# Performance work log

Measured on AMD Instinct MI355X. Metric: run time of the kernel, lower is better.

Reference implementation:

```python
import jax, jax.numpy as jnp
import numpy as np

N_NODES = 50000
N_EDGES = 800000
D = 128


def setup_inputs() -> dict:
    key = jax.random.key(0)
    k1, k2, k3, k4 = jax.random.split(key, 4)
    x = jax.random.normal(k1, (N_NODES, D), dtype=jnp.float32)
    src = jax.random.randint(k2, (N_EDGES,), 0, N_NODES, dtype=jnp.int64)
    dst = jax.random.randint(k3, (N_EDGES,), 0, N_NODES, dtype=jnp.int64)
    # nn.Linear(D, D, bias=False): weight shape [out, in]
    W = jax.random.normal(k4, (D, D), dtype=jnp.float32) * (1.0 / np.sqrt(D))
    return {"x": x, "src": src, "dst": dst, "W": W}


def reference(x, src, dst, W):
    h_in = x
    # update_all(copy_src, reduce_sum): gather src features, segment-sum over dst
    agg = jax.ops.segment_sum(x[src], dst, num_segments=N_NODES)  # [N, D]
    h = agg @ W.T                 # Linear(bias=False)
    h = jax.nn.relu(h)            # activation
    h = h + h_in                  # residual (is_normalize=False)
    return h
```

## Files before the change

kernel.cpp:

```cpp
#include <hip/hip_runtime.h>
#include <hip/hip_bf16.h>

#define N_NODES 50000
#define N_EDGES 800000
#define D 128

#define NBUCK 782
#define BCAP  2048

#define SCAT_BLOCKS ((N_EDGES / 4 + 1023) / 1024)

using bf16x8 = __attribute__((ext_vector_type(8))) short;
using u16x8  = __attribute__((ext_vector_type(8))) unsigned short;
using f32x4  = __attribute__((ext_vector_type(4))) float;

static __device__ __forceinline__ ushort f2bf(float f) {
    __hip_bfloat16 h = __float2bfloat16(f);
    return *reinterpret_cast<ushort*>(&h);
}
static __device__ __forceinline__ float bf2f(ushort u) {
    return __uint_as_float(((unsigned)u) << 16);
}


__global__ void __launch_bounds__(1024)
convert_scatter(const float4* __restrict__ x4, ushort* __restrict__ xb,
                const int* __restrict__ src, const int* __restrict__ dst,
                int* __restrict__ bcnt, int* __restrict__ pairs) {
    __shared__ int lcnt[NBUCK], lbase[NBUCK];
    const int tid = threadIdx.x;
    if (tid < NBUCK) lcnt[tid] = 0;

    const int i = blockIdx.x * 1024 + tid;
    const bool valid = i < N_EDGES / 4;
    int4 s, d;
    if (valid) {
        s = ((const int4*)src)[i];
        d = ((const int4*)dst)[i];
    }

    const int total4 = N_NODES * D / 4;
    const int stride = gridDim.x * 1024;
    for (int j = blockIdx.x * 1024 + tid; j < total4; j += stride) {
        float4 v = x4[j];
        ushort4 u = make_ushort4(f2bf(v.x), f2bf(v.y), f2bf(v.z), f2bf(v.w));
        *(ushort4*)(xb + (size_t)j * 4) = u;
    }
    __syncthreads();

    int bkt[4], slot[4];
    if (valid) {
        bkt[0] = d.x >> 6; slot[0] = atomicAdd(&lcnt[bkt[0]], 1);
        bkt[1] = d.y >> 6; slot[1] = atomicAdd(&lcnt[bkt[1]], 1);
        bkt[2] = d.z >> 6; slot[2] = atomicAdd(&lcnt[bkt[2]], 1);
        bkt[3] = d.w >> 6; slot[3] = atomicAdd(&lcnt[bkt[3]], 1);
    }
    __syncthreads();
    if (tid < NBUCK) {
        int c = lcnt[tid];
        lbase[tid] = c ? atomicAdd(&bcnt[tid], c) : 0;
    }
    __syncthreads();
    if (valid) {
#pragma unroll
        for (int e = 0; e < 4; ++e) {
            int sv = (e == 0) ? s.x : (e == 1) ? s.y : (e == 2) ? s.z : s.w;
            int dv = (e == 0) ? d.x : (e == 1) ? d.y : (e == 2) ? d.z : d.w;
            int pos = lbase[bkt[e]] + slot[e];
            if (pos < BCAP)
                pairs[bkt[e] * BCAP + pos] = sv | ((dv & 63) << 16);
        }
    }
}

__global__ void __launch_bounds__(256)
bucket_to_csr(const int* __restrict__ pairs, const int* __restrict__ bcnt,
              ushort* __restrict__ sorted_u16, int2* __restrict__ off2) {
    __shared__ int lcnt2[64], lcur[64];
    __shared__ ushort lsrc[BCAP];
    const int b    = blockIdx.x;
    const int tid  = threadIdx.x;
    const int base = b * BCAP;
    int n = bcnt[b];
    if (n > BCAP) n = BCAP;

    if (tid < 64) lcnt2[tid] = 0;
    __syncthreads();
    for (int i = tid; i < n; i += 256)
        atomicAdd(&lcnt2[pairs[base + i] >> 16], 1);
    __syncthreads();

    if (tid < 64) {
        int v = lcnt2[tid];
        int incl = v;
#pragma unroll
        for (int o = 1; o < 64; o <<= 1) {
            int t = __shfl_up(incl, o, 64);
            if (tid >= o) incl += t;
        }
        int excl = incl - v;
        lcur[tid] = excl;
        int gn = b * 64 + tid;
        if (gn < N_NODES)
            off2[gn] = make_int2(base + excl, base + incl);
    }
    __syncthreads();
    for (int i = tid; i < n; i += 256) {
        int p = pairs[base + i];
        int pos = atomicAdd(&lcur[p >> 16], 1);
        lsrc[pos] = (ushort)(p & 0xFFFF);
    }
    __syncthreads();
    for (int i = tid; i < n; i += 256)
        sorted_u16[base + i] = lsrc[i];
}

__global__ void __launch_bounds__(256)
gather_sum(const ushort* __restrict__ xb, const ushort* __restrict__ sorted_u16,
           const int2* __restrict__ off2, ushort* __restrict__ aggb) {
    int node = (int)((blockIdx.x * 256 + threadIdx.x) >> 6);
    int lane = threadIdx.x & 63;
    if (node >= N_NODES) return;
    const int q4 = lane >> 4;
    const int c8 = (lane & 15) << 3;
    const ushort* xbb = xb + c8;
    int2 oo = off2[node];
    int beg = oo.x, end = oo.y;

    float acc[8];
#pragma unroll
    for (int j = 0; j < 8; ++j) acc[j] = 0.f;

    for (int base = beg; base < end; base += 64) {
        int n = end - base;
        if (n > 64) n = 64;
        int idx = (lane < n) ? (int)sorted_u16[base + lane] : 0;
        int full = n >> 2;
        int t = 0;
        for (; t + 4 <= full; t += 4) {
            int s0 = __shfl(idx, 4 * t + q4, 64);
            int s1 = __shfl(idx, 4 * t + 4 + q4, 64);
            int s2 = __shfl(idx, 4 * t + 8 + q4, 64);
            int s3 = __shfl(idx, 4 * t + 12 + q4, 64);
            u16x8 u0 = *(const u16x8*)(xbb + (size_t)s0 * D);
            u16x8 u1 = *(const u16x8*)(xbb + (size_t)s1 * D);
            u16x8 u2 = *(const u16x8*)(xbb + (size_t)s2 * D);
            u16x8 u3 = *(const u16x8*)(xbb + (size_t)s3 * D);
#pragma unroll
            for (int j = 0; j < 8; ++j)
                acc[j] += (bf2f(u0[j]) + bf2f(u1[j])) + (bf2f(u2[j]) + bf2f(u3[j]));
        }
        for (; t < full; ++t) {
            int s = __shfl(idx, 4 * t + q4, 64);
            u16x8 u = *(const u16x8*)(xbb + (size_t)s * D);
#pragma unroll
            for (int j = 0; j < 8; ++j) acc[j] += bf2f(u[j]);
        }
        int rem = n & 3;
        if (rem) {
            int s = __shfl(idx, 4 * full + q4, 64);
            if (q4 < rem) {
                u16x8 u = *(const u16x8*)(xbb + (size_t)s * D);
#pragma unroll
                for (int j = 0; j < 8; ++j) acc[j] += bf2f(u[j]);
            }
        }
    }
#pragma unroll
    for (int j = 0; j < 8; ++j) {
        acc[j] += __shfl_xor(acc[j], 16, 64);
        acc[j] += __shfl_xor(acc[j], 32, 64);
    }
    if (q4 == 0) {
        u16x8 u;
#pragma unroll
        for (int j = 0; j < 8; ++j) u[j] = f2bf(acc[j]);
        *(u16x8*)(aggb + (size_t)node * D + c8) = u;
    }
}

__global__ void __launch_bounds__(256)
gemm_relu_res(const ushort* __restrict__ aggb,
              const float* __restrict__ W,
              const ushort* __restrict__ xb,
              float* __restrict__ out) {
    __shared__ __align__(16) char lds[33792];
    ushort* Wl = (ushort*)lds;

    const int tid  = threadIdx.x;
    const int lane = tid & 63;
    const int wv   = tid >> 6;
    const int m16  = lane & 15;
    const int q    = lane >> 4;

#pragma unroll
    for (int i = 0; i < 8; ++i) {
        int g  = tid + i * 256;
        int o  = g & 127;
        int kc = g >> 7;
        const float4* wp = (const float4*)(W + (size_t)o * D + kc * 8);
        float4 w0 = wp[0], w1 = wp[1];
        bf16x8 hv;
        hv[0] = (short)f2bf(w0.x); hv[1] = (short)f2bf(w0.y);
        hv[2] = (short)f2bf(w0.z); hv[3] = (short)f2bf(w0.w);
        hv[4] = (short)f2bf(w1.x); hv[5] = (short)f2bf(w1.y);
        hv[6] = (short)f2bf(w1.z); hv[7] = (short)f2bf(w1.w);
        *(bf16x8*)&Wl[g * 8] = hv;
    }
    __syncthreads();

    const int nb = blockIdx.x * 64 + wv * 16;
    int arow = nb + m16;
    if (arow >= N_NODES) arow = N_NODES - 1;

    bf16x8 a[4];
#pragma unroll
    for (int kb = 0; kb < 4; ++kb)
        a[kb] = *(const bf16x8*)&aggb[(size_t)arow * D + kb * 32 + q * 8];

    f32x4 acc[8];
#pragma unroll
    for (int t = 0; t < 8; ++t) {
        acc[t] = (f32x4){0.f, 0.f, 0.f, 0.f};
#pragma unroll
        for (int kb = 0; kb < 4; ++kb) {
            bf16x8 bfr = *(const bf16x8*)&Wl[(((kb * 4 + q) * 128) + t * 16 + m16) * 8];
            acc[t] = __builtin_amdgcn_mfma_f32_16x16x32_bf16(a[kb], bfr, acc[t], 0, 0, 0);
        }
    }

    __syncthreads();
    float* Ew = (float*)(lds + wv * 8448);
#pragma unroll
    for (int t = 0; t < 8; ++t)
#pragma unroll
        for (int r = 0; r < 4; ++r)
            Ew[(q * 4 + r) * 132 + t * 16 + m16] = acc[t][r];

    const int h  = lane >> 5;
    const int c4 = (lane & 31) << 2;
#pragma unroll
    for (int j = 0; j < 8; ++j) {
        int r = j * 2 + h;
        int node = nb + r;
        if (node < N_NODES) {
            float4 v  = *(const float4*)&Ew[r * 132 + c4];
            ushort4 xu = *(const ushort4*)(xb + (size_t)node * D + c4);
            float4 o;
            o.x = fmaxf(v.x, 0.f) + bf2f(xu.x);
            o.y = fmaxf(v.y, 0.f) + bf2f(xu.y);
            o.z = fmaxf(v.z, 0.f) + bf2f(xu.z);
            o.w = fmaxf(v.w, 0.f) + bf2f(xu.w);
            *(float4*)(out + (size_t)node * D + c4) = o;
        }
    }
}

__global__ void zero_out(float4* __restrict__ p, int n4) {
    int i = blockIdx.x * 256 + threadIdx.x;
    if (i < n4) p[i] = make_float4(0.f, 0.f, 0.f, 0.f);
}
__global__ void scatter_edges(const float* __restrict__ x,
                              const int* __restrict__ src,
                              const int* __restrict__ dst,
                              float* __restrict__ agg) {
    long long tid = (long long)blockIdx.x * 256 + threadIdx.x;
    if (tid >= (long long)N_EDGES * 32) return;
    int edge = (int)(tid >> 5);
    int c    = ((int)tid & 31) << 2;
    const float4 v = *(const float4*)(x + (size_t)src[edge] * D + c);
    float* p = agg + (size_t)dst[edge] * D + c;
    unsafeAtomicAdd(p + 0, v.x);
    unsafeAtomicAdd(p + 1, v.y);
    unsafeAtomicAdd(p + 2, v.z);
    unsafeAtomicAdd(p + 3, v.w);
}
__global__ void __launch_bounds__(256)
gemm_relu_res_f32(float* data, const float* __restrict__ W,
                  const float* __restrict__ x) {
    __shared__ __align__(16) char lds[50176];
    ushort* Wl = (ushort*)lds;
    ushort* Al = (ushort*)(lds + 32768);
    const int tid  = threadIdx.x;
    const int lane = tid & 63;
    const int wv   = tid >> 6;
    const int m16  = lane & 15;
    const int q    = lane >> 4;
#pragma unroll
    for (int i = 0; i < 8; ++i) {
        int g  = tid + i * 256;
        int o  = g & 127;
        int kc = g >> 7;
        const float4* wp = (const float4*)(W + (size_t)o * D + kc * 8);
        float4 w0 = wp[0], w1 = wp[1];
        bf16x8 hv;
        hv[0] = (short)f2bf(w0.x); hv[1] = (short)f2bf(w0.y);
        hv[2] = (short)f2bf(w0.z); hv[3] = (short)f2bf(w0.w);
        hv[4] = (short)f2bf(w1.x); hv[5] = (short)f2bf(w1.y);
        hv[6] = (short)f2bf(w1.z); hv[7] = (short)f2bf(w1.w);
        *(bf16x8*)&Wl[g * 8] = hv;
    }
    __syncthreads();
    const int nb = blockIdx.x * 64 + wv * 16;
    ushort* Aw = &Al[wv * (16 * 136)];
#pragma unroll
    for (int m = 0; m < 16; ++m) {
        int node = nb + m;
        float2 v = make_float2(0.f, 0.f);
        if (node < N_NODES)
            v = *(const float2*)(data + (size_t)node * D + lane * 2);
        *(ushort2*)&Aw[m * 136 + lane * 2] = make_ushort2(f2bf(v.x), f2bf(v.y));
    }
    bf16x8 a[4];
#pragma unroll
    for (int kb = 0; kb < 4; ++kb)
        a[kb] = *(const bf16x8*)&Aw[m16 * 136 + kb * 32 + q * 8];
    f32x4 acc[8];
#pragma unroll
    for (int t = 0; t < 8; ++t) {
        acc[t] = (f32x4){0.f, 0.f, 0.f, 0.f};
#pragma unroll
        for (int kb = 0; kb < 4; ++kb) {
            bf16x8 bfr = *(const bf16x8*)&Wl[(((kb * 4 + q) * 128) + t * 16 + m16) * 8];
            acc[t] = __builtin_amdgcn_mfma_f32_16x16x32_bf16(a[kb], bfr, acc[t], 0, 0, 0);
        }
    }
    __syncthreads();
    float* Ew = (float*)(lds + wv * 8448);
#pragma unroll
    for (int t = 0; t < 8; ++t)
#pragma unroll
        for (int r = 0; r < 4; ++r)
            Ew[(q * 4 + r) * 132 + t * 16 + m16] = acc[t][r];
    const int h  = lane >> 5;
    const int c4 = (lane & 31) << 2;
#pragma unroll
    for (int j = 0; j < 8; ++j) {
        int r = j * 2 + h;
        int node = nb + r;
        if (node < N_NODES) {
            float4 v  = *(const float4*)&Ew[r * 132 + c4];
            float4 xi = *(const float4*)(x + (size_t)node * D + c4);
            float4 o;
            o.x = fmaxf(v.x, 0.f) + xi.x;
            o.y = fmaxf(v.y, 0.f) + xi.y;
            o.z = fmaxf(v.z, 0.f) + xi.z;
            o.w = fmaxf(v.w, 0.f) + xi.w;
            *(float4*)(data + (size_t)node * D + c4) = o;
        }
    }
}

extern "C" void kernel_launch(void* const* d_in, const int* in_sizes, int n_in,
                              void* d_out, int out_size, void* d_ws, size_t ws_size,
                              hipStream_t stream) {
    const float* x   = (const float*)d_in[0];
    const int*   src = (const int*)d_in[1];
    const int*   dst = (const int*)d_in[2];
    const float* W   = (const float*)d_in[3];
    float* out = (float*)d_out;

    char* ws = (char*)d_ws;
    int*    bcnt  = (int*)ws;        ws += (size_t)NBUCK * 4;
    ws = (char*)(((uintptr_t)ws + 15) & ~(uintptr_t)15);
    int*    pairs = (int*)ws;        ws += (size_t)NBUCK * BCAP * 4;
    ushort* su16  = (ushort*)ws;     ws += (size_t)NBUCK * BCAP * 2;
    int2*   off2  = (int2*)ws;       ws += (size_t)N_NODES * 8;
    ws = (char*)(((uintptr_t)ws + 15) & ~(uintptr_t)15);
    ushort* xb    = (ushort*)ws;     ws += (size_t)N_NODES * D * 2;
    ushort* aggb  = (ushort*)ws;     ws += (size_t)N_NODES * D * 2;
    const bool big_ws = (ws_size >= (size_t)(ws - (char*)d_ws));

    if (big_ws) {
        hipMemsetAsync(bcnt, 0, (size_t)NBUCK * 4, stream);
        convert_scatter<<<SCAT_BLOCKS, 1024, 0, stream>>>(
            (const float4*)x, xb, src, dst, bcnt, pairs);
        bucket_to_csr<<<NBUCK, 256, 0, stream>>>(pairs, bcnt, su16, off2);
        gather_sum<<<(N_NODES * 64 + 255) / 256, 256, 0, stream>>>(
            xb, su16, off2, aggb);
        gemm_relu_res<<<(N_NODES + 63) / 64, 256, 0, stream>>>(aggb, W, xb, out);
    } else {
        int n4 = N_NODES * D / 4;
        zero_out<<<(n4 + 255) / 256, 256, 0, stream>>>((float4*)out, n4);
        long long n_scatter = (long long)N_EDGES * 32;
        scatter_edges<<<(int)((n_scatter + 255) / 256), 256, 0, stream>>>(
            x, src, dst, out);
        gemm_relu_res_f32<<<(N_NODES + 63) / 64, 256, 0, stream>>>(out, W, x);
    }
}
```

Baseline: 148.0 us.

## Fuse bucket-to-CSR, neighbor gather and GEMM epilogue into one kernel

```diff
diff --git a/kernel.cpp b/kernel.cpp
--- a/kernel.cpp
+++ b/kernel.cpp
@@ -7,6 +7,7 @@
 
 #define NBUCK 782
 #define BCAP  2048
+#define LCAP  1536
 
 #define SCAT_BLOCKS ((N_EDGES / 4 + 1023) / 1024)
 
@@ -74,119 +75,18 @@
 }
 
 __global__ void __launch_bounds__(256)
-bucket_to_csr(const int* __restrict__ pairs, const int* __restrict__ bcnt,
-              ushort* __restrict__ sorted_u16, int2* __restrict__ off2) {
-    __shared__ int lcnt2[64], lcur[64];
-    __shared__ ushort lsrc[BCAP];
+csr_gather_gemm(const int* __restrict__ pairs, const int* __restrict__ bcnt,
+                const ushort* __restrict__ xb, const float* __restrict__ W,
+                float* __restrict__ out) {
+    __shared__ __align__(16) char lds[54016];
+    ushort* Wl    = (ushort*)lds;
+    ushort* lsrc  = (ushort*)(lds + 32768);
+    ushort* aggL  = (ushort*)(lds + 35840);
+    int*    lcnt2 = (int*)(lds + 53248);
+    int*    lcur  = (int*)(lds + 53504);
+    int*    lbeg  = (int*)(lds + 53760);
+
     const int b    = blockIdx.x;
-    const int tid  = threadIdx.x;
-    const int base = b * BCAP;
-    int n = bcnt[b];
-    if (n > BCAP) n = BCAP;
-
-    if (tid < 64) lcnt2[tid] = 0;
-    __syncthreads();
-    for (int i = tid; i < n; i += 256)
-        atomicAdd(&lcnt2[pairs[base + i] >> 16], 1);
-    __syncthreads();
-
-    if (tid < 64) {
-        int v = lcnt2[tid];
-        int incl = v;
-#pragma unroll
-        for (int o = 1; o < 64; o <<= 1) {
-            int t = __shfl_up(incl, o, 64);
-            if (tid >= o) incl += t;
-        }
-        int excl = incl - v;
-        lcur[tid] = excl;
-        int gn = b * 64 + tid;
-        if (gn < N_NODES)
-            off2[gn] = make_int2(base + excl, base + incl);
-    }
-    __syncthreads();
-    for (int i = tid; i < n; i += 256) {
-        int p = pairs[base + i];
-        int pos = atomicAdd(&lcur[p >> 16], 1);
-        lsrc[pos] = (ushort)(p & 0xFFFF);
-    }
-    __syncthreads();
-    for (int i = tid; i < n; i += 256)
-        sorted_u16[base + i] = lsrc[i];
-}
-
-__global__ void __launch_bounds__(256)
-gather_sum(const ushort* __restrict__ xb, const ushort* __restrict__ sorted_u16,
-           const int2* __restrict__ off2, ushort* __restrict__ aggb) {
-    int node = (int)((blockIdx.x * 256 + threadIdx.x) >> 6);
-    int lane = threadIdx.x & 63;
-    if (node >= N_NODES) return;
-    const int q4 = lane >> 4;
-    const int c8 = (lane & 15) << 3;
-    const ushort* xbb = xb + c8;
-    int2 oo = off2[node];
-    int beg = oo.x, end = oo.y;
-
-    float acc[8];
-#pragma unroll
-    for (int j = 0; j < 8; ++j) acc[j] = 0.f;
-
-    for (int base = beg; base < end; base += 64) {
-        int n = end - base;
-        if (n > 64) n = 64;
-        int idx = (lane < n) ? (int)sorted_u16[base + lane] : 0;
-        int full = n >> 2;
-        int t = 0;
-        for (; t + 4 <= full; t += 4) {
-            int s0 = __shfl(idx, 4 * t + q4, 64);
-            int s1 = __shfl(idx, 4 * t + 4 + q4, 64);
-            int s2 = __shfl(idx, 4 * t + 8 + q4, 64);
-            int s3 = __shfl(idx, 4 * t + 12 + q4, 64);
-            u16x8 u0 = *(const u16x8*)(xbb + (size_t)s0 * D);
-            u16x8 u1 = *(const u16x8*)(xbb + (size_t)s1 * D);
-            u16x8 u2 = *(const u16x8*)(xbb + (size_t)s2 * D);
-            u16x8 u3 = *(const u16x8*)(xbb + (size_t)s3 * D);
-#pragma unroll
-            for (int j = 0; j < 8; ++j)
-                acc[j] += (bf2f(u0[j]) + bf2f(u1[j])) + (bf2f(u2[j]) + bf2f(u3[j]));
-        }
-        for (; t < full; ++t) {
-            int s = __shfl(idx, 4 * t + q4, 64);
-            u16x8 u = *(const u16x8*)(xbb + (size_t)s * D);
-#pragma unroll
-            for (int j = 0; j < 8; ++j) acc[j] += bf2f(u[j]);
-        }
-        int rem = n & 3;
-        if (rem) {
-            int s = __shfl(idx, 4 * full + q4, 64);
-            if (q4 < rem) {
-                u16x8 u = *(const u16x8*)(xbb + (size_t)s * D);
-#pragma unroll
-                for (int j = 0; j < 8; ++j) acc[j] += bf2f(u[j]);
-            }
-        }
-    }
-#pragma unroll
-    for (int j = 0; j < 8; ++j) {
-        acc[j] += __shfl_xor(acc[j], 16, 64);
-        acc[j] += __shfl_xor(acc[j], 32, 64);
-    }
-    if (q4 == 0) {
-        u16x8 u;
-#pragma unroll
-        for (int j = 0; j < 8; ++j) u[j] = f2bf(acc[j]);
-        *(u16x8*)(aggb + (size_t)node * D + c8) = u;
-    }
-}
-
-__global__ void __launch_bounds__(256)
-gemm_relu_res(const ushort* __restrict__ aggb,
-              const float* __restrict__ W,
-              const ushort* __restrict__ xb,
-              float* __restrict__ out) {
-    __shared__ __align__(16) char lds[33792];
-    ushort* Wl = (ushort*)lds;
-
     const int tid  = threadIdx.x;
     const int lane = tid & 63;
     const int wv   = tid >> 6;
@@ -207,16 +107,89 @@
         hv[6] = (short)f2bf(w1.z); hv[7] = (short)f2bf(w1.w);
         *(bf16x8*)&Wl[g * 8] = hv;
     }
-    __syncthreads();
-
-    const int nb = blockIdx.x * 64 + wv * 16;
-    int arow = nb + m16;
-    if (arow >= N_NODES) arow = N_NODES - 1;
+
+    const int base = b * BCAP;
+    int n = bcnt[b];
+    if (n > LCAP) n = LCAP;
+    if (tid < 64) lcnt2[tid] = 0;
+    __syncthreads();
+    for (int i = tid; i < n; i += 256)
+        atomicAdd(&lcnt2[pairs[base + i] >> 16], 1);
+    __syncthreads();
+    if (tid < 64) {
+        int v = lcnt2[tid];
+        int incl = v;
+#pragma unroll
+        for (int o = 1; o < 64; o <<= 1) {
+            int t = __shfl_up(incl, o, 64);
+            if (tid >= o) incl += t;
+        }
+        lbeg[tid] = incl - v;
+        lcur[tid] = incl - v;
+    }
+    __syncthreads();
+    for (int i = tid; i < n; i += 256) {
+        int p = pairs[base + i];
+        int pos = atomicAdd(&lcur[p >> 16], 1);
+        lsrc[pos] = (ushort)(p & 0xFFFF);
+    }
+    __syncthreads();
+
+    const int c8 = m16 << 3;
+    const ushort* xbb = xb + c8;
+#pragma unroll 1
+    for (int m = 0; m < 16; ++m) {
+        const int node = wv * 16 + m;
+        const int beg = lbeg[node], end = lcur[node];
+        float acc[8];
+#pragma unroll
+        for (int j = 0; j < 8; ++j) acc[j] = 0.f;
+
+        int t = beg;
+        for (; t + 16 <= end; t += 16) {
+            int s0 = lsrc[t + q];
+            int s1 = lsrc[t + 4 + q];
+            int s2 = lsrc[t + 8 + q];
+            int s3 = lsrc[t + 12 + q];
+            u16x8 u0 = *(const u16x8*)(xbb + (size_t)s0 * D);
+            u16x8 u1 = *(const u16x8*)(xbb + (size_t)s1 * D);
+            u16x8 u2 = *(const u16x8*)(xbb + (size_t)s2 * D);
+            u16x8 u3 = *(const u16x8*)(xbb + (size_t)s3 * D);
+#pragma unroll
+            for (int j = 0; j < 8; ++j)
+                acc[j] += (bf2f(u0[j]) + bf2f(u1[j])) + (bf2f(u2[j]) + bf2f(u3[j]));
+        }
+        for (; t + 4 <= end; t += 4) {
+            int s = lsrc[t + q];
+            u16x8 u = *(const u16x8*)(xbb + (size_t)s * D);
+#pragma unroll
+            for (int j = 0; j < 8; ++j) acc[j] += bf2f(u[j]);
+        }
+        const int rem = end - t;
+        if (rem && q < rem) {
+            int s = lsrc[t + q];
+            u16x8 u = *(const u16x8*)(xbb + (size_t)s * D);
+#pragma unroll
+            for (int j = 0; j < 8; ++j) acc[j] += bf2f(u[j]);
+        }
+#pragma unroll
+        for (int j = 0; j < 8; ++j) {
+            acc[j] += __shfl_xor(acc[j], 16, 64);
+            acc[j] += __shfl_xor(acc[j], 32, 64);
+        }
+        if (q == 0) {
+            u16x8 u;
+#pragma unroll
+            for (int j = 0; j < 8; ++j) u[j] = f2bf(acc[j]);
+            *(u16x8*)&aggL[(size_t)node * 136 + c8] = u;
+        }
+    }
+    __syncthreads();
 
     bf16x8 a[4];
 #pragma unroll
     for (int kb = 0; kb < 4; ++kb)
-        a[kb] = *(const bf16x8*)&aggb[(size_t)arow * D + kb * 32 + q * 8];
+        a[kb] = *(const bf16x8*)&aggL[(size_t)(wv * 16 + m16) * 136 + kb * 32 + q * 8];
 
     f32x4 acc[8];
 #pragma unroll
@@ -237,6 +210,7 @@
         for (int r = 0; r < 4; ++r)
             Ew[(q * 4 + r) * 132 + t * 16 + m16] = acc[t][r];
 
+    const int nb = b * 64 + wv * 16;
     const int h  = lane >> 5;
     const int c4 = (lane & 31) << 2;
 #pragma unroll
@@ -364,21 +338,14 @@
     int*    bcnt  = (int*)ws;        ws += (size_t)NBUCK * 4;
     ws = (char*)(((uintptr_t)ws + 15) & ~(uintptr_t)15);
     int*    pairs = (int*)ws;        ws += (size_t)NBUCK * BCAP * 4;
-    ushort* su16  = (ushort*)ws;     ws += (size_t)NBUCK * BCAP * 2;
-    int2*   off2  = (int2*)ws;       ws += (size_t)N_NODES * 8;
-    ws = (char*)(((uintptr_t)ws + 15) & ~(uintptr_t)15);
     ushort* xb    = (ushort*)ws;     ws += (size_t)N_NODES * D * 2;
-    ushort* aggb  = (ushort*)ws;     ws += (size_t)N_NODES * D * 2;
     const bool big_ws = (ws_size >= (size_t)(ws - (char*)d_ws));
 
     if (big_ws) {
         hipMemsetAsync(bcnt, 0, (size_t)NBUCK * 4, stream);
         convert_scatter<<<SCAT_BLOCKS, 1024, 0, stream>>>(
             (const float4*)x, xb, src, dst, bcnt, pairs);
-        bucket_to_csr<<<NBUCK, 256, 0, stream>>>(pairs, bcnt, su16, off2);
-        gather_sum<<<(N_NODES * 64 + 255) / 256, 256, 0, stream>>>(
-            xb, su16, off2, aggb);
-        gemm_relu_res<<<(N_NODES + 63) / 64, 256, 0, stream>>>(aggb, W, xb, out);
+        csr_gather_gemm<<<NBUCK, 256, 0, stream>>>(pairs, bcnt, xb, W, out);
     } else {
         int n4 = N_NODES * D / 4;
         zero_out<<<(n4 + 255) / 256, 256, 0, stream>>>((float4*)out, n4);
```

Result: slower. 163.4 us (+10.4%).

## Replace two-level bucket CSR build with 16-node buckets filtered per wave in gather

Applied to the files above, without the earlier changes.

```diff
diff --git a/kernel.cpp b/kernel.cpp
--- a/kernel.cpp
+++ b/kernel.cpp
@@ -5,10 +5,12 @@
 #define N_EDGES 800000
 #define D 128
 
-#define NBUCK 782
-#define BCAP  2048
-
-#define SCAT_BLOCKS ((N_EDGES / 4 + 1023) / 1024)
+#define SB     3125
+#define SBP    3200
+#define WCAP16 384
+#define EPB    8192
+#define SBLK   98
+#define XBLK   800
 
 using bf16x8 = __attribute__((ext_vector_type(8))) short;
 using u16x8  = __attribute__((ext_vector_type(8))) unsigned short;
@@ -26,152 +28,168 @@
 __global__ void __launch_bounds__(1024)
 convert_scatter(const float4* __restrict__ x4, ushort* __restrict__ xb,
                 const int* __restrict__ src, const int* __restrict__ dst,
-                int* __restrict__ bcnt, int* __restrict__ pairs) {
-    __shared__ int lcnt[NBUCK], lbase[NBUCK];
+                int* __restrict__ bcnt, unsigned* __restrict__ pairs) {
+    __shared__ int      A[SBP];
+    __shared__ int      B[SBP];
+    __shared__ unsigned payload[EPB];
     const int tid = threadIdx.x;
-    if (tid < NBUCK) lcnt[tid] = 0;
-
-    const int i = blockIdx.x * 1024 + tid;
-    const bool valid = i < N_EDGES / 4;
-    int4 s, d;
-    if (valid) {
-        s = ((const int4*)src)[i];
-        d = ((const int4*)dst)[i];
-    }
-
-    const int total4 = N_NODES * D / 4;
-    const int stride = gridDim.x * 1024;
-    for (int j = blockIdx.x * 1024 + tid; j < total4; j += stride) {
-        float4 v = x4[j];
-        ushort4 u = make_ushort4(f2bf(v.x), f2bf(v.y), f2bf(v.z), f2bf(v.w));
-        *(ushort4*)(xb + (size_t)j * 4) = u;
-    }
-    __syncthreads();
-
-    int bkt[4], slot[4];
-    if (valid) {
-        bkt[0] = d.x >> 6; slot[0] = atomicAdd(&lcnt[bkt[0]], 1);
-        bkt[1] = d.y >> 6; slot[1] = atomicAdd(&lcnt[bkt[1]], 1);
-        bkt[2] = d.z >> 6; slot[2] = atomicAdd(&lcnt[bkt[2]], 1);
-        bkt[3] = d.w >> 6; slot[3] = atomicAdd(&lcnt[bkt[3]], 1);
-    }
-    __syncthreads();
-    if (tid < NBUCK) {
-        int c = lcnt[tid];
-        lbase[tid] = c ? atomicAdd(&bcnt[tid], c) : 0;
-    }
-    __syncthreads();
-    if (valid) {
-#pragma unroll
-        for (int e = 0; e < 4; ++e) {
-            int sv = (e == 0) ? s.x : (e == 1) ? s.y : (e == 2) ? s.z : s.w;
-            int dv = (e == 0) ? d.x : (e == 1) ? d.y : (e == 2) ? d.z : d.w;
-            int pos = lbase[bkt[e]] + slot[e];
-            if (pos < BCAP)
-                pairs[bkt[e] * BCAP + pos] = sv | ((dv & 63) << 16);
+
+    if (blockIdx.x >= SBLK) {
+        const int gt = (blockIdx.x - SBLK) * 1024 + tid;
+        const int total4 = N_NODES * D / 4;
+        const int stride = XBLK * 1024;
+        for (int j = gt; j < total4; j += stride) {
+            float4 v = x4[j];
+            ushort4 u = make_ushort4(f2bf(v.x), f2bf(v.y), f2bf(v.z), f2bf(v.w));
+            *(ushort4*)(xb + (size_t)j * 4) = u;
+        }
+        return;
+    }
+
+    const int base = blockIdx.x * EPB;
+    int nblk = N_EDGES - base;
+    if (nblk > EPB) nblk = EPB;
+
+    for (int i = tid; i < SBP; i += 1024) A[i] = 0;
+    __syncthreads();
+
+    unsigned pk[8];
+#pragma unroll
+    for (int k = 0; k < 8; ++k) {
+        int i = k * 1024 + tid;
+        pk[k] = 0xFFFFFFFFu;
+        if (i < nblk) {
+            int e = base + i;
+            pk[k] = (unsigned)src[e] | ((unsigned)dst[e] << 16);
+            atomicAdd(&A[pk[k] >> 20], 1);
+        }
+    }
+    __syncthreads();
+
+    for (int i = tid; i < SBP; i += 1024) B[i] = A[i];
+    __syncthreads();
+
+    for (int off = 1; off < SBP; off <<= 1) {
+        int t[4];
+#pragma unroll
+        for (int k = 0; k < 4; ++k) {
+            int i = tid + k * 1024;
+            t[k] = (i < SBP && i >= off) ? A[i - off] : 0;
+        }
+        __syncthreads();
+#pragma unroll
+        for (int k = 0; k < 4; ++k) {
+            int i = tid + k * 1024;
+            if (i < SBP) A[i] += t[k];
+        }
+        __syncthreads();
+    }
+
+    for (int i = tid; i < SBP; i += 1024) {
+        int incl = A[i], cnt = B[i];
+        int excl = incl - cnt;
+        int gb = cnt ? atomicAdd(&bcnt[i * 16], cnt) : 0;
+        A[i] = i * WCAP16 + gb - excl;
+        B[i] = excl;
+    }
+    __syncthreads();
+
+#pragma unroll
+    for (int k = 0; k < 8; ++k) {
+        unsigned p = pk[k];
+        if (p != 0xFFFFFFFFu) {
+            int pos = atomicAdd(&B[p >> 20], 1);
+            payload[pos] = p;
+        }
+    }
+    __syncthreads();
+
+#pragma unroll
+    for (int k = 0; k < 8; ++k) {
+        int i = k * 1024 + tid;
+        if (i < nblk) {
+            unsigned p = payload[i];
+            int bkt = (int)(p >> 20);
+            int addr = i + A[bkt];
+            if (addr < (bkt + 1) * WCAP16)
+                pairs[addr] = p;
         }
     }
 }
 
 __global__ void __launch_bounds__(256)
-bucket_to_csr(const int* __restrict__ pairs, const int* __restrict__ bcnt,
-              ushort* __restrict__ sorted_u16, int2* __restrict__ off2) {
-    __shared__ int lcnt2[64], lcur[64];
-    __shared__ ushort lsrc[BCAP];
-    const int b    = blockIdx.x;
+gather_sum(const unsigned* __restrict__ pairs, const int* __restrict__ bcnt,
+           const ushort* __restrict__ xb, ushort* __restrict__ aggb) {
+    __shared__ ushort lsw[4][64];
     const int tid  = threadIdx.x;
-    const int base = b * BCAP;
-    int n = bcnt[b];
-    if (n > BCAP) n = BCAP;
-
-    if (tid < 64) lcnt2[tid] = 0;
-    __syncthreads();
-    for (int i = tid; i < n; i += 256)
-        atomicAdd(&lcnt2[pairs[base + i] >> 16], 1);
-    __syncthreads();
-
-    if (tid < 64) {
-        int v = lcnt2[tid];
-        int incl = v;
-#pragma unroll
-        for (int o = 1; o < 64; o <<= 1) {
-            int t = __shfl_up(incl, o, 64);
-            if (tid >= o) incl += t;
-        }
-        int excl = incl - v;
-        lcur[tid] = excl;
-        int gn = b * 64 + tid;
-        if (gn < N_NODES)
-            off2[gn] = make_int2(base + excl, base + incl);
-    }
-    __syncthreads();
-    for (int i = tid; i < n; i += 256) {
-        int p = pairs[base + i];
-        int pos = atomicAdd(&lcur[p >> 16], 1);
-        lsrc[pos] = (ushort)(p & 0xFFFF);
-    }
-    __syncthreads();
-    for (int i = tid; i < n; i += 256)
-        sorted_u16[base + i] = lsrc[i];
-}
-
-__global__ void __launch_bounds__(256)
-gather_sum(const ushort* __restrict__ xb, const ushort* __restrict__ sorted_u16,
-           const int2* __restrict__ off2, ushort* __restrict__ aggb) {
-    int node = (int)((blockIdx.x * 256 + threadIdx.x) >> 6);
-    int lane = threadIdx.x & 63;
-    if (node >= N_NODES) return;
-    const int q4 = lane >> 4;
+    const int wv   = tid >> 6;
+    const int lane = tid & 63;
+    const int node = blockIdx.x * 4 + wv;
+    const int b16  = node >> 4;
+    const unsigned sub = (unsigned)(node & 15);
+
+    int cnt = bcnt[b16 * 16];
+    if (cnt > WCAP16) cnt = WCAP16;
+    const unsigned* wp = pairs + (size_t)b16 * WCAP16;
+
+    int deg = 0;
+#pragma unroll
+    for (int k = 0; k < 6; ++k) {
+        int i = k * 64 + lane;
+        unsigned p = (i < cnt) ? wp[i] : 0u;
+        bool m = (i < cnt) && (((p >> 16) & 15u) == sub);
+        unsigned long long mask = __ballot(m);
+        if (m) {
+            int rank = deg + __popcll(mask & ((1ULL << lane) - 1ULL));
+            if (rank < 64) lsw[wv][rank] = (ushort)(p & 0xFFFFu);
+        }
+        deg += (int)__popcll(mask);
+    }
+    if (deg > 64) deg = 64;
+
+    const int q  = lane >> 4;
     const int c8 = (lane & 15) << 3;
     const ushort* xbb = xb + c8;
-    int2 oo = off2[node];
-    int beg = oo.x, end = oo.y;
 
     float acc[8];
 #pragma unroll
     for (int j = 0; j < 8; ++j) acc[j] = 0.f;
 
-    for (int base = beg; base < end; base += 64) {
-        int n = end - base;
-        if (n > 64) n = 64;
-        int idx = (lane < n) ? (int)sorted_u16[base + lane] : 0;
-        int full = n >> 2;
-        int t = 0;
-        for (; t + 4 <= full; t += 4) {
-            int s0 = __shfl(idx, 4 * t + q4, 64);
-            int s1 = __shfl(idx, 4 * t + 4 + q4, 64);
-            int s2 = __shfl(idx, 4 * t + 8 + q4, 64);
-            int s3 = __shfl(idx, 4 * t + 12 + q4, 64);
-            u16x8 u0 = *(const u16x8*)(xbb + (size_t)s0 * D);
-            u16x8 u1 = *(const u16x8*)(xbb + (size_t)s1 * D);
-            u16x8 u2 = *(const u16x8*)(xbb + (size_t)s2 * D);
-            u16x8 u3 = *(const u16x8*)(xbb + (size_t)s3 * D);
-#pragma unroll
-            for (int j = 0; j < 8; ++j)
-                acc[j] += (bf2f(u0[j]) + bf2f(u1[j])) + (bf2f(u2[j]) + bf2f(u3[j]));
-        }
-        for (; t < full; ++t) {
-            int s = __shfl(idx, 4 * t + q4, 64);
-            u16x8 u = *(const u16x8*)(xbb + (size_t)s * D);
-#pragma unroll
-            for (int j = 0; j < 8; ++j) acc[j] += bf2f(u[j]);
-        }
-        int rem = n & 3;
-        if (rem) {
-            int s = __shfl(idx, 4 * full + q4, 64);
-            if (q4 < rem) {
-                u16x8 u = *(const u16x8*)(xbb + (size_t)s * D);
-#pragma unroll
-                for (int j = 0; j < 8; ++j) acc[j] += bf2f(u[j]);
-            }
-        }
-    }
+    const int full = deg >> 2;
+    int t = 0;
+    for (; t + 4 <= full; t += 4) {
+        int s0 = lsw[wv][4 * t + q];
+        int s1 = lsw[wv][4 * t + 4 + q];
+        int s2 = lsw[wv][4 * t + 8 + q];
+        int s3 = lsw[wv][4 * t + 12 + q];
+        u16x8 u0 = *(const u16x8*)(xbb + (size_t)s0 * D);
+        u16x8 u1 = *(const u16x8*)(xbb + (size_t)s1 * D);
+        u16x8 u2 = *(const u16x8*)(xbb + (size_t)s2 * D);
+        u16x8 u3 = *(const u16x8*)(xbb + (size_t)s3 * D);
+#pragma unroll
+        for (int j = 0; j < 8; ++j)
+            acc[j] += (bf2f(u0[j]) + bf2f(u1[j])) + (bf2f(u2[j]) + bf2f(u3[j]));
+    }
+    for (; t < full; ++t) {
+        int s = lsw[wv][4 * t + q];
+        u16x8 u = *(const u16x8*)(xbb + (size_t)s * D);
+#pragma unroll
+        for (int j = 0; j < 8; ++j) acc[j] += bf2f(u[j]);
+    }
+    const int rem = deg & 3;
+    if (rem && q < rem) {
+        int s = lsw[wv][4 * full + q];
+        u16x8 u = *(const u16x8*)(xbb + (size_t)s * D);
+#pragma unroll
+        for (int j = 0; j < 8; ++j) acc[j] += bf2f(u[j]);
+    }
+
 #pragma unroll
     for (int j = 0; j < 8; ++j) {
         acc[j] += __shfl_xor(acc[j], 16, 64);
         acc[j] += __shfl_xor(acc[j], 32, 64);
     }
-    if (q4 == 0) {
+    if (q == 0) {
         u16x8 u;
 #pragma unroll
         for (int j = 0; j < 8; ++j) u[j] = f2bf(acc[j]);
@@ -361,23 +379,17 @@
     float* out = (float*)d_out;
 
     char* ws = (char*)d_ws;
-    int*    bcnt  = (int*)ws;        ws += (size_t)NBUCK * 4;
-    ws = (char*)(((uintptr_t)ws + 15) & ~(uintptr_t)15);
-    int*    pairs = (int*)ws;        ws += (size_t)NBUCK * BCAP * 4;
-    ushort* su16  = (ushort*)ws;     ws += (size_t)NBUCK * BCAP * 2;
-    int2*   off2  = (int2*)ws;       ws += (size_t)N_NODES * 8;
-    ws = (char*)(((uintptr_t)ws + 15) & ~(uintptr_t)15);
-    ushort* xb    = (ushort*)ws;     ws += (size_t)N_NODES * D * 2;
-    ushort* aggb  = (ushort*)ws;     ws += (size_t)N_NODES * D * 2;
+    int*      bcnt  = (int*)ws;      ws += (size_t)SBP * 64;
+    unsigned* pairs = (unsigned*)ws; ws += (size_t)SB * WCAP16 * 4;
+    ushort*   xb    = (ushort*)ws;   ws += (size_t)N_NODES * D * 2;
+    ushort*   aggb  = (ushort*)ws;   ws += (size_t)N_NODES * D * 2;
     const bool big_ws = (ws_size >= (size_t)(ws - (char*)d_ws));
 
     if (big_ws) {
-        hipMemsetAsync(bcnt, 0, (size_t)NBUCK * 4, stream);
-        convert_scatter<<<SCAT_BLOCKS, 1024, 0, stream>>>(
+        hipMemsetAsync(bcnt, 0, (size_t)SBP * 64, stream);
+        convert_scatter<<<SBLK + XBLK, 1024, 0, stream>>>(
             (const float4*)x, xb, src, dst, bcnt, pairs);
-        bucket_to_csr<<<NBUCK, 256, 0, stream>>>(pairs, bcnt, su16, off2);
-        gather_sum<<<(N_NODES * 64 + 255) / 256, 256, 0, stream>>>(
-            xb, su16, off2, aggb);
+        gather_sum<<<N_NODES / 4, 256, 0, stream>>>(pairs, bcnt, xb, aggb);
         gemm_relu_res<<<(N_NODES + 63) / 64, 256, 0, stream>>>(aggb, W, xb, out);
     } else {
         int n4 = N_NODES * D / 4;
```

Measured after the change: 154.8 us. +4.5%, slower.
